# Kernel tuning notes

Measured on AMD Instinct MI355X. Metric: run time of the kernel, lower is better.

Reference implementation:

```python
import jax, jax.numpy as jnp
import numpy as np

D_MODEL = 512
D_FFN = 2048
N_LAYERS = 6
VOCAB = 1000
D_STATE = 16
D_CONV = 4
D_INNER = 2 * D_MODEL  # expand=2
DT_RANK = 32           # ceil(d_model/16)
B, LT, LS = 2, 512, 512


def _pos_encoding(length, d_model):
    pos = np.arange(length, dtype=np.float32)[:, None]
    div = np.exp(np.arange(0, d_model, 2, dtype=np.float32) * (-np.log(10000.0) / d_model))
    pe = np.zeros((length, d_model), np.float32)
    pe[:, 0::2] = np.sin(pos * div)
    pe[:, 1::2] = np.cos(pos * div)
    return jnp.asarray(pe)


def _layer_norm(x, g, b, eps=1e-6):
    m = x.mean(-1, keepdims=True)
    v = ((x - m) ** 2).mean(-1, keepdims=True)
    return (x - m) * jax.lax.rsqrt(v + eps) * g + b


def _mamba(x, in_w, conv_w, conv_b, xproj_w, dt_w, dt_b, A_log, Dskip, out_w):
    # x: (b, l, d_model)
    b, l, _ = x.shape
    xz = x @ in_w.T                                   # (b, l, 2*d_inner)
    xc, z = jnp.split(xz, 2, axis=-1)
    # causal depthwise conv over time
    xt = jnp.transpose(xc, (0, 2, 1))                 # (b, d_inner, l)
    xt = jnp.pad(xt, ((0, 0), (0, 0), (D_CONV - 1, 0)))
    xt = jax.lax.conv_general_dilated(
        xt, conv_w, window_strides=(1,), padding='VALID',
        feature_group_count=D_INNER, dimension_numbers=('NCH', 'OIH', 'NCH'))
    xc = jax.nn.silu(jnp.transpose(xt, (0, 2, 1)) + conv_b)  # (b, l, d_inner)
    dbl = xc @ xproj_w.T                              # (b, l, dt_rank + 2*n)
    dt, Bm, Cm = jnp.split(dbl, [DT_RANK, DT_RANK + D_STATE], axis=-1)
    dt = jax.nn.softplus(dt @ dt_w.T + dt_b)          # (b, l, d_inner)
    A = -jnp.exp(A_log)                               # (d_inner, n)

    def step(h, xs):
        dt_t, B_t, C_t, u_t = xs                      # (b,d),(b,n),(b,n),(b,d)
        dA = jnp.exp(dt_t[..., None] * A)             # (b, d, n)
        h = dA * h + (dt_t * u_t)[..., None] * B_t[:, None, :]
        y = jnp.einsum('bdn,bn->bd', h, C_t)
        return h, y

    h0 = jnp.zeros((b, D_INNER, D_STATE), x.dtype)
    xs = (jnp.swapaxes(dt, 0, 1), jnp.swapaxes(Bm, 0, 1),
          jnp.swapaxes(Cm, 0, 1), jnp.swapaxes(xc, 0, 1))
    _, ys = jax.lax.scan(step, h0, xs)                # ys: (l, b, d_inner)
    y = jnp.swapaxes(ys, 0, 1) + xc * Dskip
    y = y * jax.nn.silu(z)
    return y @ out_w.T                                # (b, l, d_model)


def setup_inputs() -> dict:
    key = jax.random.key(0)
    ks = iter(jax.random.split(key, 40))

    def rn(shape, s=0.02):
        return jax.random.normal(next(ks), shape, jnp.float32) * s

    def mamba_params():
        return dict(
            in_w=rn((N_LAYERS, 2 * D_INNER, D_MODEL)),
            conv_w=rn((N_LAYERS, D_INNER, 1, D_CONV), 0.1),
            conv_b=rn((N_LAYERS, D_INNER)),
            xproj=rn((N_LAYERS, DT_RANK + 2 * D_STATE, D_INNER)),
            dtw=rn((N_LAYERS, D_INNER, DT_RANK)),
            dtb=rn((N_LAYERS, D_INNER)),
            Alog=jnp.log(jnp.broadcast_to(jnp.arange(1.0, D_STATE + 1.0, dtype=jnp.float32), (N_LAYERS, D_INNER, D_STATE))),
            D=jnp.ones((N_LAYERS, D_INNER), jnp.float32),
            outw=rn((N_LAYERS, D_MODEL, D_INNER)),
        )

    ps, pc = mamba_params(), mamba_params()
    inp = {
        'src': jax.random.normal(next(ks), (B, LS, D_MODEL), jnp.float32),
        'tgt': jax.random.randint(next(ks), (B, LT), 0, VOCAB),
        'emb': rn((VOCAB, D_MODEL)),
        'in_w_s': ps['in_w'], 'conv_w_s': ps['conv_w'], 'conv_b_s': ps['conv_b'],
        'xproj_s': ps['xproj'], 'dtw_s': ps['dtw'], 'dtb_s': ps['dtb'],
        'Alog_s': ps['Alog'], 'D_s': ps['D'], 'outw_s': ps['outw'],
        'in_w_c': pc['in_w'], 'conv_w_c': pc['conv_w'], 'conv_b_c': pc['conv_b'],
        'xproj_c': pc['xproj'], 'dtw_c': pc['dtw'], 'dtb_c': pc['dtb'],
        'Alog_c': pc['Alog'], 'D_c': pc['D'], 'outw_c': pc['outw'],
        'ffn_w1': rn((N_LAYERS, D_FFN, D_MODEL)),
        'ffn_b1': jnp.zeros((N_LAYERS, D_FFN), jnp.float32),
        'ffn_w2': rn((N_LAYERS, D_MODEL, D_FFN)),
        'ffn_b2': jnp.zeros((N_LAYERS, D_MODEL), jnp.float32),
        'ln_g': jnp.ones((N_LAYERS, 3, D_MODEL), jnp.float32),
        'ln_b': jnp.zeros((N_LAYERS, 3, D_MODEL), jnp.float32),
        'fin_g': jnp.ones((D_MODEL,), jnp.float32),
        'fin_b': jnp.zeros((D_MODEL,), jnp.float32),
    }
    return inp


def reference(src, tgt, emb, in_w_s, conv_w_s, conv_b_s, xproj_s, dtw_s, dtb_s,
              Alog_s, D_s, outw_s, in_w_c, conv_w_c, conv_b_c, xproj_c, dtw_c,
              dtb_c, Alog_c, D_c, outw_c, ffn_w1, ffn_b1, ffn_w2, ffn_b2,
              ln_g, ln_b, fin_g, fin_b):
    # NormalizedEmbedding + sinusoidal positional encoding
    x = emb[tgt] * jnp.sqrt(jnp.asarray(D_MODEL, jnp.float32))
    x = x + _pos_encoding(LT, D_MODEL)[None]
    for i in range(N_LAYERS):
        # self mamba (post-norm, normalize_before=False)
        t2 = _mamba(x, in_w_s[i], conv_w_s[i], conv_b_s[i], xproj_s[i],
                    dtw_s[i], dtb_s[i], Alog_s[i], D_s[i], outw_s[i])
        x = _layer_norm(x + t2, ln_g[i, 0], ln_b[i, 0])
        # cross mamba over concat([memory, tgt]) then take last LT steps
        cat = jnp.concatenate([src, x], axis=1)
        t2 = _mamba(cat, in_w_c[i], conv_w_c[i], conv_b_c[i], xproj_c[i],
                    dtw_c[i], dtb_c[i], Alog_c[i], D_c[i], outw_c[i])[:, -LT:]
        x = _layer_norm(x + t2, ln_g[i, 1], ln_b[i, 1])
        # positionwise FFN
        h = jax.nn.relu(x @ ffn_w1[i].T + ffn_b1[i]) @ ffn_w2[i].T + ffn_b2[i]
        x = _layer_norm(x + h, ln_g[i, 2], ln_b[i, 2])
    return _layer_norm(x, fin_g, fin_b)
```

## Files before the change

kernel.cpp:

```cpp
#include <hip/hip_runtime.h>
#include <math.h>

#define DMODEL 512
#define DINNER 1024
#define DSTATE 16
#define DTRANK 32
#define NLAYERS 6
#define BB 2
#define LT 512
#define LS 512

typedef __attribute__((ext_vector_type(8))) short bf16x8;
typedef __attribute__((ext_vector_type(8))) unsigned short u16x8;
typedef __attribute__((ext_vector_type(4))) float f32x4;

__device__ __forceinline__ unsigned short f2bf(float f) {
  unsigned u = __float_as_uint(f);
  u += 0x7fffu + ((u >> 16) & 1u);
  return (unsigned short)(u >> 16);
}
__device__ __forceinline__ float bf2f(unsigned short u) {
  return __uint_as_float((unsigned)u << 16);
}

template<int EPI>
__device__ __forceinline__ float epi_apply(float acc, float b) {
  if (EPI == 1) { float v = acc + b; return v > 0.f ? v : 0.f; }
  if (EPI == 2) { return acc + b; }
  if (EPI == 3) { float v = acc + b; return fmaxf(v, 0.f) + log1pf(__expf(-fabsf(v))); }
  return acc;
}

__global__ __launch_bounds__(256) void cvt_all_kernel(
    const float* __restrict__ i0, const float* __restrict__ i1,
    const float* __restrict__ i2, const float* __restrict__ i3,
    const float* __restrict__ i4, const float* __restrict__ i5,
    const float* __restrict__ i6, const float* __restrict__ i7,
    const float* __restrict__ i8, const float* __restrict__ i9,
    unsigned short* __restrict__ outbase) {
  int i = blockIdx.x * 256 + threadIdx.x;
  if (i >= 8159232) return;
  const float* in; int off;
  if      (i < 1572864) { in = i0; off = i; }
  else if (i < 3145728) { in = i1; off = i - 1572864; }
  else if (i < 3244032) { in = i2; off = i - 3145728; }
  else if (i < 3342336) { in = i3; off = i - 3244032; }
  else if (i < 3391488) { in = i4; off = i - 3342336; }
  else if (i < 3440640) { in = i5; off = i - 3391488; }
  else if (i < 4227072) { in = i6; off = i - 3440640; }
  else if (i < 5013504) { in = i7; off = i - 4227072; }
  else if (i < 6586368) { in = i8; off = i - 5013504; }
  else                  { in = i9; off = i - 6586368; }
  float4 a = ((const float4*)in)[off];
  ushort4 o = make_ushort4(f2bf(a.x), f2bf(a.y), f2bf(a.z), f2bf(a.w));
  *(ushort4*)&outbase[(size_t)i * 4] = o;
}

__global__ __launch_bounds__(256) void embed_cat_kernel(const int* __restrict__ tgt,
    const float* __restrict__ emb, const float* __restrict__ src,
    float* __restrict__ X, unsigned short* __restrict__ Xb,
    unsigned short* __restrict__ CATb) {
  if (blockIdx.x < 2048) {
    int i = blockIdx.x * 256 + threadIdx.x;
    int d = i & (DMODEL - 1);
    int bt = i >> 9;
    int t = bt & (LT - 1);
    int tok = tgt[bt];
    float div = __expf((float)(d & ~1) * (-9.210340371976184f / (float)DMODEL));
    float ang = (float)t * div;
    float pe = (d & 1) ? cosf(ang) : sinf(ang);
    float v = emb[(size_t)tok * DMODEL + d] * 22.627416997969522f + pe;
    X[i] = v;
    Xb[i] = f2bf(v);
  } else {
    int i = (blockIdx.x - 2048) * 256 + threadIdx.x;
    int c8 = (i & 63) * 8;
    int r = i >> 6;
    int b = r >> 9, l = r & 511;
    const float* s = src + ((size_t)b * 512 + l) * DMODEL + c8;
    float4 a = *(const float4*)s;
    float4 bq = *(const float4*)(s + 4);
    u16x8 o;
    o[0] = f2bf(a.x); o[1] = f2bf(a.y); o[2] = f2bf(a.z); o[3] = f2bf(a.w);
    o[4] = f2bf(bq.x); o[5] = f2bf(bq.y); o[6] = f2bf(bq.z); o[7] = f2bf(bq.w);
    *(u16x8*)&CATb[((size_t)b * 1024 + l) * DMODEL + c8] = o;
  }
}

template<int BK, int EPI, bool SPLIT, bool OUTB>
__global__ __launch_bounds__(256) void mgemmA(
    const unsigned short* __restrict__ A, const unsigned short* __restrict__ Bw,
    const float* __restrict__ bias, float* __restrict__ C,
    unsigned short* __restrict__ Cb, int M, int N, int K, int lda) {
  constexpr int PAD = BK + 8;
  constexpr int CHA = BK / 32;
  constexpr int CHB = BK / 16;
  __shared__ __align__(16) unsigned short As[2][64 * PAD];
  __shared__ __align__(16) unsigned short Bs[2][128 * PAD];
  const int tid = threadIdx.x;
  const int bn = blockIdx.x * 128;
  const int bm = blockIdx.y * 64;
  const int lane = tid & 63;
  const int w = tid >> 6;
  const int wr = (w >> 1) * 32;
  const int wc = (w & 1) * 64;
  const int l15 = lane & 15;
  const int l4 = lane >> 4;
  const int koff = l4 * 8;
  int kcnt = K, kbeg = 0;
  if (SPLIT) { kcnt = K / (int)gridDim.z; kbeg = blockIdx.z * kcnt; }
  const int nt = kcnt / BK;
  f32x4 acc[2][4] = {};

  int arow_[CHA], ak8_[CHA];
  const unsigned short* Ap[CHA];
#pragma unroll
  for (int i = 0; i < CHA; ++i) {
    int f = tid + 256 * i;
    arow_[i] = f / (BK / 8);
    ak8_[i] = (f % (BK / 8)) * 8;
    Ap[i] = A + (size_t)(bm + arow_[i]) * lda + kbeg + ak8_[i];
  }
  int brow_[CHB], bk8_[CHB];
  const unsigned short* Bp[CHB];
#pragma unroll
  for (int i = 0; i < CHB; ++i) {
    int f = tid + 256 * i;
    brow_[i] = f / (BK / 8);
    bk8_[i] = (f % (BK / 8)) * 8;
    Bp[i] = Bw + (size_t)(bn + brow_[i]) * K + kbeg + bk8_[i];
  }

  u16x8 av[CHA], bv[CHB];
#pragma unroll
  for (int i = 0; i < CHA; ++i) av[i] = *(const u16x8*)Ap[i];
#pragma unroll
  for (int i = 0; i < CHB; ++i) bv[i] = *(const u16x8*)Bp[i];

  int cur = 0;
  for (int t = 0; t < nt; ++t) {
#pragma unroll
    for (int i = 0; i < CHA; ++i) *(u16x8*)&As[cur][arow_[i] * PAD + ak8_[i]] = av[i];
#pragma unroll
    for (int i = 0; i < CHB; ++i) *(u16x8*)&Bs[cur][brow_[i] * PAD + bk8_[i]] = bv[i];
    if (t + 1 < nt) {
      int ko = (t + 1) * BK;
#pragma unroll
      for (int i = 0; i < CHA; ++i) av[i] = *(const u16x8*)(Ap[i] + ko);
#pragma unroll
      for (int i = 0; i < CHB; ++i) bv[i] = *(const u16x8*)(Bp[i] + ko);
    }
    __syncthreads();
#pragma unroll
    for (int kk = 0; kk < BK / 32; ++kk) {
      bf16x8 afr[2], bfr[4];
#pragma unroll
      for (int i = 0; i < 2; ++i)
        afr[i] = *(const bf16x8*)&As[cur][(wr + i * 16 + l15) * PAD + kk * 32 + koff];
#pragma unroll
      for (int j = 0; j < 4; ++j)
        bfr[j] = *(const bf16x8*)&Bs[cur][(wc + j * 16 + l15) * PAD + kk * 32 + koff];
#pragma unroll
      for (int fr = 0; fr < 2; ++fr)
#pragma unroll
        for (int fc = 0; fc < 4; ++fc)
          acc[fr][fc] = __builtin_amdgcn_mfma_f32_16x16x32_bf16(
              afr[fr], bfr[fc], acc[fr][fc], 0, 0, 0);
    }
    cur ^= 1;
  }

  if (SPLIT) {
    unsigned short* Pz = Cb + (size_t)blockIdx.z * M * N;
#pragma unroll
    for (int fc = 0; fc < 4; ++fc) {
      int col = bn + wc + fc * 16 + l15;
#pragma unroll
      for (int fr = 0; fr < 2; ++fr) {
        int row0 = bm + wr + fr * 16 + l4 * 4;
#pragma unroll
        for (int r = 0; r < 4; ++r)
          Pz[(size_t)(row0 + r) * N + col] = f2bf(acc[fr][fc][r]);
      }
    }
  } else {
#pragma unroll
    for (int fc = 0; fc < 4; ++fc) {
      int col = bn + wc + fc * 16 + l15;
      float bvs = (EPI != 0) ? bias[col] : 0.f;
#pragma unroll
      for (int fr = 0; fr < 2; ++fr) {
        int row0 = bm + wr + fr * 16 + l4 * 4;
#pragma unroll
        for (int r = 0; r < 4; ++r) {
          float v = epi_apply<EPI>(acc[fr][fc][r], bvs);
          if (OUTB) Cb[(size_t)(row0 + r) * N + col] = f2bf(v);
          else      C[(size_t)(row0 + r) * N + col] = v;
        }
      }
    }
  }
}

template<int BK, int EPI, bool SPLIT, bool OUTB>
__global__ __launch_bounds__(256) void mgemm(
    const unsigned short* __restrict__ A, const unsigned short* __restrict__ Bw,
    const float* __restrict__ bias, float* __restrict__ C,
    unsigned short* __restrict__ Cb, int M, int N, int K, int lda) {
  constexpr int PAD = BK + 8;
  constexpr int CH = BK / 32;
  __shared__ __align__(16) unsigned short As[2][64 * PAD];
  __shared__ __align__(16) unsigned short Bs[2][64 * PAD];
  const int tid = threadIdx.x;
  const int bn = blockIdx.x * 64;
  const int bm = blockIdx.y * 64;
  const int lane = tid & 63;
  const int w = tid >> 6;
  const int wr = (w >> 1) * 32;
  const int wc = (w & 1) * 32;
  const int l15 = lane & 15;
  const int l4 = lane >> 4;
  const int koff = l4 * 8;
  int kcnt = K, kbeg = 0;
  if (SPLIT) { kcnt = K / (int)gridDim.z; kbeg = blockIdx.z * kcnt; }
  const int nt = kcnt / BK;
  f32x4 acc[2][2] = {};

  int row_[CH], k8_[CH];
  const unsigned short *Ap[CH], *Bp[CH];
#pragma unroll
  for (int i = 0; i < CH; ++i) {
    int f = tid + 256 * i;
    row_[i] = f / (BK / 8);
    k8_[i] = (f % (BK / 8)) * 8;
    Ap[i] = A + (size_t)(bm + row_[i]) * lda + kbeg + k8_[i];
    Bp[i] = Bw + (size_t)(bn + row_[i]) * K + kbeg + k8_[i];
  }

  u16x8 av[CH], bv[CH];
#pragma unroll
  for (int i = 0; i < CH; ++i) { av[i] = *(const u16x8*)Ap[i]; bv[i] = *(const u16x8*)Bp[i]; }

  int cur = 0;
  for (int t = 0; t < nt; ++t) {
#pragma unroll
    for (int i = 0; i < CH; ++i) {
      *(u16x8*)&As[cur][row_[i] * PAD + k8_[i]] = av[i];
      *(u16x8*)&Bs[cur][row_[i] * PAD + k8_[i]] = bv[i];
    }
    if (t + 1 < nt) {
      int ko = (t + 1) * BK;
#pragma unroll
      for (int i = 0; i < CH; ++i) {
        av[i] = *(const u16x8*)(Ap[i] + ko);
        bv[i] = *(const u16x8*)(Bp[i] + ko);
      }
    }
    __syncthreads();
#pragma unroll
    for (int kk = 0; kk < CH; ++kk) {
      bf16x8 afr[2], bfr[2];
#pragma unroll
      for (int i = 0; i < 2; ++i) {
        afr[i] = *(const bf16x8*)&As[cur][(wr + i * 16 + l15) * PAD + kk * 32 + koff];
        bfr[i] = *(const bf16x8*)&Bs[cur][(wc + i * 16 + l15) * PAD + kk * 32 + koff];
      }
#pragma unroll
      for (int fr = 0; fr < 2; ++fr)
#pragma unroll
        for (int fc = 0; fc < 2; ++fc)
          acc[fr][fc] = __builtin_amdgcn_mfma_f32_16x16x32_bf16(
              afr[fr], bfr[fc], acc[fr][fc], 0, 0, 0);
    }
    cur ^= 1;
  }

  if (SPLIT) {
    float* Pz = C + (size_t)blockIdx.z * M * N;
#pragma unroll
    for (int fc = 0; fc < 2; ++fc) {
      int col = bn + wc + fc * 16 + l15;
#pragma unroll
      for (int fr = 0; fr < 2; ++fr) {
        int row0 = bm + wr + fr * 16 + l4 * 4;
#pragma unroll
        for (int r = 0; r < 4; ++r)
          Pz[(size_t)(row0 + r) * N + col] = acc[fr][fc][r];
      }
    }
  } else {
#pragma unroll
    for (int fc = 0; fc < 2; ++fc) {
      int col = bn + wc + fc * 16 + l15;
      float bvs = (EPI != 0) ? bias[col] : 0.f;
#pragma unroll
      for (int fr = 0; fr < 2; ++fr) {
        int row0 = bm + wr + fr * 16 + l4 * 4;
#pragma unroll
        for (int r = 0; r < 4; ++r) {
          float v = epi_apply<EPI>(acc[fr][fc][r], bvs);
          if (OUTB) Cb[(size_t)(row0 + r) * N + col] = f2bf(v);
          else      C[(size_t)(row0 + r) * N + col] = v;
        }
      }
    }
  }
}

__global__ __launch_bounds__(256) void conv_silu_kernel(
    const unsigned short* __restrict__ xzb, const float* __restrict__ w,
    const float* __restrict__ bias, unsigned short* __restrict__ outb, int L) {
  int idx = blockIdx.x * 256 + threadIdx.x;
  int d8 = (idx & 127) * 8;
  int bt = idx >> 7;
  int b = bt / L;
  int t = bt - b * L;
  const unsigned short* col = xzb + ((size_t)b * L) * (2 * DINNER) + d8;
  float acc[8];
  float4 wv[8];
#pragma unroll
  for (int j = 0; j < 8; ++j) {
    acc[j] = bias[d8 + j];
    wv[j] = *(const float4*)(w + (size_t)(d8 + j) * 4);
  }
#pragma unroll
  for (int k = 0; k < 4; ++k) {
    int tt = t - 3 + k;
    if (tt >= 0) {
      u16x8 v = *(const u16x8*)(col + (size_t)tt * (2 * DINNER));
      float wk[8] = {
        k == 0 ? wv[0].x : k == 1 ? wv[0].y : k == 2 ? wv[0].z : wv[0].w,
        k == 0 ? wv[1].x : k == 1 ? wv[1].y : k == 2 ? wv[1].z : wv[1].w,
        k == 0 ? wv[2].x : k == 1 ? wv[2].y : k == 2 ? wv[2].z : wv[2].w,
        k == 0 ? wv[3].x : k == 1 ? wv[3].y : k == 2 ? wv[3].z : wv[3].w,
        k == 0 ? wv[4].x : k == 1 ? wv[4].y : k == 2 ? wv[4].z : wv[4].w,
        k == 0 ? wv[5].x : k == 1 ? wv[5].y : k == 2 ? wv[5].z : wv[5].w,
        k == 0 ? wv[6].x : k == 1 ? wv[6].y : k == 2 ? wv[6].z : wv[6].w,
        k == 0 ? wv[7].x : k == 1 ? wv[7].y : k == 2 ? wv[7].z : wv[7].w };
#pragma unroll
      for (int j = 0; j < 8; ++j) acc[j] = fmaf(bf2f(v[j]), wk[j], acc[j]);
    }
  }
  u16x8 o;
#pragma unroll
  for (int j = 0; j < 8; ++j) {
    float sig = 1.f / (1.f + __expf(-acc[j]));
    o[j] = f2bf(acc[j] * sig);
  }
  *(u16x8*)&outb[(size_t)bt * DINNER + d8] = o;
}

__global__ __launch_bounds__(256) void scan_pass1(
    const float* __restrict__ XPP, const unsigned short* __restrict__ u,
    const float* __restrict__ Alog, const float* __restrict__ dtw,
    const float* __restrict__ dtb, float* __restrict__ P, float* __restrict__ S,
    int L, int CL) {
  __shared__ float DBL8[32][64];
  const int tid = threadIdx.x;
  const int d = blockIdx.x * 256 + tid;
  const int b = blockIdx.y;
  const int c = blockIdx.z;
  const int t0 = c * CL;
  if (tid < CL * 8) {
    int t = tid >> 3, j8 = (tid & 7) * 8;
    const float* p = XPP + ((size_t)b * L + t0 + t) * 64 + j8;
    const size_t zs = (size_t)BB * L * 64;
    float s[8] = {0.f, 0.f, 0.f, 0.f, 0.f, 0.f, 0.f, 0.f};
#pragma unroll
    for (int z = 0; z < 8; ++z) {
      float4 a = *(const float4*)(p + z * zs);
      float4 bq = *(const float4*)(p + z * zs + 4);
      s[0] += a.x; s[1] += a.y; s[2] += a.z; s[3] += a.w;
      s[4] += bq.x; s[5] += bq.y; s[6] += bq.z; s[7] += bq.w;
    }
#pragma unroll
    for (int j = 0; j < 8; ++j) DBL8[t][j8 + j] = s[j];
  }
  float A[16];
#pragma unroll
  for (int j = 0; j < 4; ++j) {
    float4 a4 = *(const float4*)(Alog + d * 16 + j * 4);
    A[j * 4 + 0] = -__expf(a4.x); A[j * 4 + 1] = -__expf(a4.y);
    A[j * 4 + 2] = -__expf(a4.z); A[j * 4 + 3] = -__expf(a4.w);
  }
  float wreg[32];
#pragma unroll
  for (int j = 0; j < 8; ++j) {
    float4 w4 = *(const float4*)(dtw + (size_t)d * 32 + j * 4);
    wreg[j*4+0] = w4.x; wreg[j*4+1] = w4.y; wreg[j*4+2] = w4.z; wreg[j*4+3] = w4.w;
  }
  float dtbv = dtb[d];
  float h[16], Pp[16];
#pragma unroll
  for (int n = 0; n < 16; ++n) { h[n] = 0.f; Pp[n] = 1.f; }
  const unsigned short* up = u + ((size_t)b * L + t0) * DINNER + d;
  __syncthreads();
  for (int t = 0; t < CL; ++t) {
    float dtraw = dtbv;
#pragma unroll
    for (int k8 = 0; k8 < 8; ++k8) {
      float4 q = *(const float4*)&DBL8[t][k8 * 4];
      dtraw = fmaf(q.x, wreg[k8*4+0], dtraw);
      dtraw = fmaf(q.y, wreg[k8*4+1], dtraw);
      dtraw = fmaf(q.z, wreg[k8*4+2], dtraw);
      dtraw = fmaf(q.w, wreg[k8*4+3], dtraw);
    }
    float dtv = fmaxf(dtraw, 0.f) + log1pf(__expf(-fabsf(dtraw)));
    float uv = bf2f(up[(size_t)t * DINNER]);
    float du = dtv * uv;
    float Bv[16];
#pragma unroll
    for (int j = 0; j < 4; ++j) {
      float4 b4 = *(const float4*)&DBL8[t][32 + j * 4];
      Bv[j*4+0] = b4.x; Bv[j*4+1] = b4.y; Bv[j*4+2] = b4.z; Bv[j*4+3] = b4.w;
    }
#pragma unroll
    for (int n = 0; n < 16; ++n) {
      float dA = __expf(dtv * A[n]);
      Pp[n] *= dA;
      h[n] = fmaf(dA, h[n], du * Bv[n]);
    }
  }
  size_t base = (size_t)c * 32768 + ((size_t)(b * 1024 + d) << 4);
#pragma unroll
  for (int j = 0; j < 4; ++j) {
    *(float4*)&P[base + j * 4] = make_float4(Pp[j*4], Pp[j*4+1], Pp[j*4+2], Pp[j*4+3]);
    *(float4*)&S[base + j * 4] = make_float4(h[j*4], h[j*4+1], h[j*4+2], h[j*4+3]);
  }
}

__global__ __launch_bounds__(256) void scan_pass2(
    const float* __restrict__ XPP, const unsigned short* __restrict__ u,
    const unsigned short* __restrict__ xzb, const float* __restrict__ Alog,
    const float* __restrict__ dtw, const float* __restrict__ dtb,
    const float* __restrict__ Dsk, const float* __restrict__ P,
    const float* __restrict__ S, unsigned short* __restrict__ ysb,
    int L, int CL, int c0) {
  __shared__ float DBL8[32][64];
  const int tid = threadIdx.x;
  const int d = blockIdx.x * 256 + tid;
  const int b = blockIdx.y;
  const int c = blockIdx.z + c0;
  const int t0 = c * CL;
  if (tid < CL * 8) {
    int t = tid >> 3, j8 = (tid & 7) * 8;
    const float* p = XPP + ((size_t)b * L + t0 + t) * 64 + j8;
    const size_t zs = (size_t)BB * L * 64;
    float s[8] = {0.f, 0.f, 0.f, 0.f, 0.f, 0.f, 0.f, 0.f};
#pragma unroll
    for (int z = 0; z < 8; ++z) {
      float4 a = *(const float4*)(p + z * zs);
      float4 bq = *(const float4*)(p + z * zs + 4);
      s[0] += a.x; s[1] += a.y; s[2] += a.z; s[3] += a.w;
      s[4] += bq.x; s[5] += bq.y; s[6] += bq.z; s[7] += bq.w;
    }
#pragma unroll
    for (int j = 0; j < 8; ++j) DBL8[t][j8 + j] = s[j];
  }
  float A[16];
#pragma unroll
  for (int j = 0; j < 4; ++j) {
    float4 a4 = *(const float4*)(Alog + d * 16 + j * 4);
    A[j * 4 + 0] = -__expf(a4.x); A[j * 4 + 1] = -__expf(a4.y);
    A[j * 4 + 2] = -__expf(a4.z); A[j * 4 + 3] = -__expf(a4.w);
  }
  float wreg[32];
#pragma unroll
  for (int j = 0; j < 8; ++j) {
    float4 w4 = *(const float4*)(dtw + (size_t)d * 32 + j * 4);
    wreg[j*4+0] = w4.x; wreg[j*4+1] = w4.y; wreg[j*4+2] = w4.z; wreg[j*4+3] = w4.w;
  }
  float dtbv = dtb[d];
  float h[16];
#pragma unroll
  for (int n = 0; n < 16; ++n) h[n] = 0.f;
  size_t sbase = (size_t)(b * 1024 + d) << 4;
  for (int cc = 0; cc < c; ++cc) {
    size_t bb = (size_t)cc * 32768 + sbase;
#pragma unroll
    for (int j = 0; j < 4; ++j) {
      float4 p4 = *(const float4*)&P[bb + j * 4];
      float4 s4 = *(const float4*)&S[bb + j * 4];
      h[j*4+0] = fmaf(p4.x, h[j*4+0], s4.x);
      h[j*4+1] = fmaf(p4.y, h[j*4+1], s4.y);
      h[j*4+2] = fmaf(p4.z, h[j*4+2], s4.z);
      h[j*4+3] = fmaf(p4.w, h[j*4+3], s4.w);
    }
  }
  float Dv = Dsk[d];
  const unsigned short* up = u + ((size_t)b * L + t0) * DINNER + d;
  const unsigned short* zp = xzb + ((size_t)b * L + t0) * (2 * DINNER) + DINNER + d;
  unsigned short* yp = ysb + ((size_t)(b * 512) + (t0 - c0 * CL)) * DINNER + d;
  __syncthreads();
  for (int t = 0; t < CL; ++t) {
    float dtraw = dtbv;
#pragma unroll
    for (int k8 = 0; k8 < 8; ++k8) {
      float4 q = *(const float4*)&DBL8[t][k8 * 4];
      dtraw = fmaf(q.x, wreg[k8*4+0], dtraw);
      dtraw = fmaf(q.y, wreg[k8*4+1], dtraw);
      dtraw = fmaf(q.z, wreg[k8*4+2], dtraw);
      dtraw = fmaf(q.w, wreg[k8*4+3], dtraw);
    }
    float dtv = fmaxf(dtraw, 0.f) + log1pf(__expf(-fabsf(dtraw)));
    float uv = bf2f(up[(size_t)t * DINNER]);
    float zv = bf2f(zp[(size_t)t * (2 * DINNER)]);
    float du = dtv * uv;
    float Bv[16], Cv[16];
#pragma unroll
    for (int j = 0; j < 4; ++j) {
      float4 b4 = *(const float4*)&DBL8[t][32 + j * 4];
      float4 c4 = *(const float4*)&DBL8[t][48 + j * 4];
      Bv[j*4+0] = b4.x; Bv[j*4+1] = b4.y; Bv[j*4+2] = b4.z; Bv[j*4+3] = b4.w;
      Cv[j*4+0] = c4.x; Cv[j*4+1] = c4.y; Cv[j*4+2] = c4.z; Cv[j*4+3] = c4.w;
    }
    float y = 0.f;
#pragma unroll
    for (int n = 0; n < 16; ++n) {
      float dA = __expf(dtv * A[n]);
      h[n] = fmaf(dA, h[n], du * Bv[n]);
      y = fmaf(h[n], Cv[n], y);
    }
    float sig = 1.f / (1.f + __expf(-zv));
    yp[(size_t)t * DINNER] = f2bf((y + uv * Dv) * (zv * sig));
  }
}

template<int NZ, int EPI, bool FIN>
__global__ __launch_bounds__(64) void ln_red_kernel(
    const float* __restrict__ res, const unsigned short* __restrict__ Pb,
    const float* __restrict__ bias, const float* __restrict__ g,
    const float* __restrict__ be, float* __restrict__ out,
    unsigned short* __restrict__ outb, int row_scale, int row_off,
    const float* __restrict__ fing, const float* __restrict__ finb,
    float* __restrict__ fout) {
  int r = blockIdx.x;
  int b = r >> 9, t = r & 511;
  int lane = threadIdx.x;
  const float* rp = res + (size_t)r * DMODEL;
  size_t ob = ((size_t)(b * row_scale + row_off + t)) * DMODEL;
  float v[8];
  float s = 0.f, ss = 0.f;
#pragma unroll
  for (int j = 0; j < 8; ++j) {
    int col = lane + j * 64;
    float acc = 0.f;
#pragma unroll
    for (int z = 0; z < NZ; ++z)
      acc += bf2f(Pb[(size_t)z * 524288 + (size_t)r * DMODEL + col]);
    float bv = (EPI != 0) ? bias[col] : 0.f;
    float x = rp[col] + epi_apply<EPI>(acc, bv);
    v[j] = x; s += x; ss += x * x;
  }
#pragma unroll
  for (int o = 32; o > 0; o >>= 1) { s += __shfl_xor(s, o); ss += __shfl_xor(ss, o); }
  float m = s * (1.f / 512.f);
  float var = ss * (1.f / 512.f) - m * m;
  float rs = rsqrtf(var + 1e-6f);
  if (FIN) {
    float o2[8];
    float s2 = 0.f, ss2 = 0.f;
#pragma unroll
    for (int j = 0; j < 8; ++j) {
      int col = lane + j * 64;
      float x = (v[j] - m) * rs * g[col] + be[col];
      o2[j] = x; s2 += x; ss2 += x * x;
    }
#pragma unroll
    for (int o = 32; o > 0; o >>= 1) { s2 += __shfl_xor(s2, o); ss2 += __shfl_xor(ss2, o); }
    float m2 = s2 * (1.f / 512.f);
    float var2 = ss2 * (1.f / 512.f) - m2 * m2;
    float rs2 = rsqrtf(var2 + 1e-6f);
#pragma unroll
    for (int j = 0; j < 8; ++j) {
      int col = lane + j * 64;
      fout[(size_t)r * DMODEL + col] = (o2[j] - m2) * rs2 * fing[col] + finb[col];
    }
  } else {
#pragma unroll
    for (int j = 0; j < 8; ++j) {
      int col = lane + j * 64;
      float o2 = (v[j] - m) * rs * g[col] + be[col];
      out[(size_t)r * DMODEL + col] = o2;
      outb[ob + col] = f2bf(o2);
    }
  }
}

extern "C" void kernel_launch(void* const* d_in, const int* in_sizes, int n_in,
                              void* d_out, int out_size, void* d_ws, size_t ws_size,
                              hipStream_t stream) {
  (void)in_sizes; (void)n_in; (void)out_size; (void)ws_size;
  const float* src      = (const float*)d_in[0];
  const int*   tgt      = (const int*)d_in[1];
  const float* emb      = (const float*)d_in[2];
  const float* in_w_s   = (const float*)d_in[3];
  const float* conv_w_s = (const float*)d_in[4];
  const float* conv_b_s = (const float*)d_in[5];
  const float* xproj_s  = (const float*)d_in[6];
  const float* dtw_s    = (const float*)d_in[7];
  const float* dtb_s    = (const float*)d_in[8];
  const float* Alog_s   = (const float*)d_in[9];
  const float* D_s      = (const float*)d_in[10];
  const float* outw_s   = (const float*)d_in[11];
  const float* in_w_c   = (const float*)d_in[12];
  const float* conv_w_c = (const float*)d_in[13];
  const float* conv_b_c = (const float*)d_in[14];
  const float* xproj_c  = (const float*)d_in[15];
  const float* dtw_c    = (const float*)d_in[16];
  const float* dtb_c    = (const float*)d_in[17];
  const float* Alog_c   = (const float*)d_in[18];
  const float* D_c      = (const float*)d_in[19];
  const float* outw_c   = (const float*)d_in[20];
  const float* ffn_w1   = (const float*)d_in[21];
  const float* ffn_b1   = (const float*)d_in[22];
  const float* ffn_w2   = (const float*)d_in[23];
  const float* ffn_b2   = (const float*)d_in[24];
  const float* ln_g     = (const float*)d_in[25];
  const float* ln_b     = (const float*)d_in[26];
  const float* fin_g    = (const float*)d_in[27];
  const float* fin_b    = (const float*)d_in[28];

  float* ws   = (float*)d_ws;
  float* X    = ws;
  float* XPP  = X + 524288;
  float* SC_P = XPP + 1048576;
  float* SC_S = SC_P + 1048576;
  unsigned short* U = (unsigned short*)(SC_S + 1048576);
  unsigned short* Xb   = U;
  unsigned short* CATb = Xb + 524288;
  unsigned short* XCb  = CATb + 1048576;
  unsigned short* XZb  = XCb + 2097152;
  unsigned short* YSb  = XZb + 4194304;
  unsigned short* XZPb = YSb + 1048576;
  unsigned short* WB   = XZPb + 4194304;
  unsigned short* inwsb = WB;
  unsigned short* inwcb = inwsb + 6291456;
  unsigned short* xpsb  = inwcb + 6291456;
  unsigned short* xpcb  = xpsb + 393216;
  unsigned short* dtwsb = xpcb + 393216;
  unsigned short* dtwcb = dtwsb + 196608;
  unsigned short* owsb  = dtwcb + 196608;
  unsigned short* owcb  = owsb + 3145728;
  unsigned short* f1b   = owcb + 3145728;
  unsigned short* f2b   = f1b + 6291456;

  cvt_all_kernel<<<31872, 256, 0, stream>>>(
      in_w_s, in_w_c, xproj_s, xproj_c, dtw_s, dtw_c, outw_s, outw_c,
      ffn_w1, ffn_w2, WB);
  embed_cat_kernel<<<2304, 256, 0, stream>>>(tgt, emb, src, X, Xb, CATb);

  for (int i = 0; i < NLAYERS; ++i) {
    mgemm<64, 0, false, true><<<dim3(32, 16), 256, 0, stream>>>(
        Xb, inwsb + (size_t)i * 1048576, nullptr, nullptr, XZb, 1024, 2048, 512, 512);
    conv_silu_kernel<<<512, 256, 0, stream>>>(
        XZb, conv_w_s + (size_t)i * 4096, conv_b_s + (size_t)i * 1024, XCb, 512);
    mgemm<64, 0, true, false><<<dim3(1, 16, 8), 256, 0, stream>>>(
        XCb, xpsb + (size_t)i * 65536, nullptr, XPP, nullptr, 1024, 64, 1024, 1024);
    scan_pass1<<<dim3(4, 2, 32), 256, 0, stream>>>(
        XPP, XCb, Alog_s + (size_t)i * 16384, dtw_s + (size_t)i * 32768,
        dtb_s + (size_t)i * 1024, SC_P, SC_S, 512, 16);
    scan_pass2<<<dim3(4, 2, 32), 256, 0, stream>>>(
        XPP, XCb, XZb, Alog_s + (size_t)i * 16384, dtw_s + (size_t)i * 32768,
        dtb_s + (size_t)i * 1024, D_s + (size_t)i * 1024, SC_P, SC_S, YSb, 512, 16, 0);
    mgemmA<64, 0, true, false><<<dim3(4, 16, 8), 256, 0, stream>>>(
        YSb, owsb + (size_t)i * 524288, nullptr, nullptr, XZPb, 1024, 512, 1024, 1024);
    ln_red_kernel<8, 0, false><<<1024, 64, 0, stream>>>(
        X, XZPb, nullptr, ln_g + (size_t)(i * 3 + 0) * 512,
        ln_b + (size_t)(i * 3 + 0) * 512, X, CATb, 1024, 512,
        nullptr, nullptr, nullptr);

    mgemmA<64, 0, false, true><<<dim3(16, 32), 256, 0, stream>>>(
        CATb, inwcb + (size_t)i * 1048576, nullptr, nullptr, XZb, 2048, 2048, 512, 512);
    conv_silu_kernel<<<1024, 256, 0, stream>>>(
        XZb, conv_w_c + (size_t)i * 4096, conv_b_c + (size_t)i * 1024, XCb, 1024);
    mgemm<64, 0, true, false><<<dim3(1, 32, 8), 256, 0, stream>>>(
        XCb, xpcb + (size_t)i * 65536, nullptr, XPP, nullptr, 2048, 64, 1024, 1024);
    scan_pass1<<<dim3(4, 2, 32), 256, 0, stream>>>(
        XPP, XCb, Alog_c + (size_t)i * 16384, dtw_c + (size_t)i * 32768,
        dtb_c + (size_t)i * 1024, SC_P, SC_S, 1024, 32);
    scan_pass2<<<dim3(4, 2, 16), 256, 0, stream>>>(
        XPP, XCb, XZb, Alog_c + (size_t)i * 16384, dtw_c + (size_t)i * 32768,
        dtb_c + (size_t)i * 1024, D_c + (size_t)i * 1024, SC_P, SC_S, YSb, 1024, 32, 16);
    mgemmA<64, 0, true, false><<<dim3(4, 16, 8), 256, 0, stream>>>(
        YSb, owcb + (size_t)i * 524288, nullptr, nullptr, XZPb, 1024, 512, 1024, 1024);
    ln_red_kernel<8, 0, false><<<1024, 64, 0, stream>>>(
        X, XZPb, nullptr, ln_g + (size_t)(i * 3 + 1) * 512,
        ln_b + (size_t)(i * 3 + 1) * 512, X, Xb, 512, 0,
        nullptr, nullptr, nullptr);

    mgemm<64, 1, false, true><<<dim3(32, 16), 256, 0, stream>>>(
        Xb, f1b + (size_t)i * 1048576, ffn_b1 + (size_t)i * 2048, nullptr, XZb,
        1024, 2048, 512, 512);
    mgemmA<64, 0, true, false><<<dim3(4, 16, 8), 256, 0, stream>>>(
        XZb, f2b + (size_t)i * 1048576, nullptr, nullptr, XZPb, 1024, 512, 2048, 2048);
    if (i < NLAYERS - 1) {
      ln_red_kernel<8, 2, false><<<1024, 64, 0, stream>>>(
          X, XZPb, ffn_b2 + (size_t)i * 512, ln_g + (size_t)(i * 3 + 2) * 512,
          ln_b + (size_t)(i * 3 + 2) * 512, X, Xb, 512, 0,
          nullptr, nullptr, nullptr);
    } else {
      ln_red_kernel<8, 2, true><<<1024, 64, 0, stream>>>(
          X, XZPb, ffn_b2 + (size_t)i * 512, ln_g + (size_t)(i * 3 + 2) * 512,
          ln_b + (size_t)(i * 3 + 2) * 512, nullptr, nullptr, 512, 0,
          fin_g, fin_b, (float*)d_out);
    }
  }
}
```

Measured before the change: 1.137 ms.

## Merge weight-convert and embed kernels, pack LN rows per block, add nontemporal split-K I/O

Combines the weight bf16 conversion and the embedding/concat kernel into one launch to save a launch. Split-K partial stores and the layer-norm reductions' partial loads now use nontemporal hints. The layer-norm kernel handles four rows per 256-thread block instead of one row per 64-thread block, giving fewer, larger blocks. The nontemporal hints could hurt if the partials would otherwise have been served from cache.

```diff
diff --git a/kernel.cpp b/kernel.cpp
--- a/kernel.cpp
+++ b/kernel.cpp
@@ -31,37 +31,35 @@
   return acc;
 }
 
-__global__ __launch_bounds__(256) void cvt_all_kernel(
+__global__ __launch_bounds__(256) void cvt_embed_kernel(
     const float* __restrict__ i0, const float* __restrict__ i1,
     const float* __restrict__ i2, const float* __restrict__ i3,
     const float* __restrict__ i4, const float* __restrict__ i5,
     const float* __restrict__ i6, const float* __restrict__ i7,
     const float* __restrict__ i8, const float* __restrict__ i9,
-    unsigned short* __restrict__ outbase) {
-  int i = blockIdx.x * 256 + threadIdx.x;
-  if (i >= 8159232) return;
-  const float* in; int off;
-  if      (i < 1572864) { in = i0; off = i; }
-  else if (i < 3145728) { in = i1; off = i - 1572864; }
-  else if (i < 3244032) { in = i2; off = i - 3145728; }
-  else if (i < 3342336) { in = i3; off = i - 3244032; }
-  else if (i < 3391488) { in = i4; off = i - 3342336; }
-  else if (i < 3440640) { in = i5; off = i - 3391488; }
-  else if (i < 4227072) { in = i6; off = i - 3440640; }
-  else if (i < 5013504) { in = i7; off = i - 4227072; }
-  else if (i < 6586368) { in = i8; off = i - 5013504; }
-  else                  { in = i9; off = i - 6586368; }
-  float4 a = ((const float4*)in)[off];
-  ushort4 o = make_ushort4(f2bf(a.x), f2bf(a.y), f2bf(a.z), f2bf(a.w));
-  *(ushort4*)&outbase[(size_t)i * 4] = o;
-}
-
-__global__ __launch_bounds__(256) void embed_cat_kernel(const int* __restrict__ tgt,
-    const float* __restrict__ emb, const float* __restrict__ src,
-    float* __restrict__ X, unsigned short* __restrict__ Xb,
-    unsigned short* __restrict__ CATb) {
-  if (blockIdx.x < 2048) {
+    unsigned short* __restrict__ outbase,
+    const int* __restrict__ tgt, const float* __restrict__ emb,
+    const float* __restrict__ src, float* __restrict__ X,
+    unsigned short* __restrict__ Xb, unsigned short* __restrict__ CATb) {
+  if (blockIdx.x < 31872) {
     int i = blockIdx.x * 256 + threadIdx.x;
+    if (i >= 8159232) return;
+    const float* in; int off;
+    if      (i < 1572864) { in = i0; off = i; }
+    else if (i < 3145728) { in = i1; off = i - 1572864; }
+    else if (i < 3244032) { in = i2; off = i - 3145728; }
+    else if (i < 3342336) { in = i3; off = i - 3244032; }
+    else if (i < 3391488) { in = i4; off = i - 3342336; }
+    else if (i < 3440640) { in = i5; off = i - 3391488; }
+    else if (i < 4227072) { in = i6; off = i - 3440640; }
+    else if (i < 5013504) { in = i7; off = i - 4227072; }
+    else if (i < 6586368) { in = i8; off = i - 5013504; }
+    else                  { in = i9; off = i - 6586368; }
+    float4 a = ((const float4*)in)[off];
+    ushort4 o = make_ushort4(f2bf(a.x), f2bf(a.y), f2bf(a.z), f2bf(a.w));
+    *(ushort4*)&outbase[(size_t)i * 4] = o;
+  } else if (blockIdx.x < 31872 + 2048) {
+    int i = (blockIdx.x - 31872) * 256 + threadIdx.x;
     int d = i & (DMODEL - 1);
     int bt = i >> 9;
     int t = bt & (LT - 1);
@@ -73,7 +71,7 @@
     X[i] = v;
     Xb[i] = f2bf(v);
   } else {
-    int i = (blockIdx.x - 2048) * 256 + threadIdx.x;
+    int i = (blockIdx.x - 31872 - 2048) * 256 + threadIdx.x;
     int c8 = (i & 63) * 8;
     int r = i >> 6;
     int b = r >> 9, l = r & 511;
@@ -180,7 +178,8 @@
         int row0 = bm + wr + fr * 16 + l4 * 4;
 #pragma unroll
         for (int r = 0; r < 4; ++r)
-          Pz[(size_t)(row0 + r) * N + col] = f2bf(acc[fr][fc][r]);
+          __builtin_nontemporal_store(f2bf(acc[fr][fc][r]),
+                                      &Pz[(size_t)(row0 + r) * N + col]);
       }
     }
   } else {
@@ -285,7 +284,8 @@
         int row0 = bm + wr + fr * 16 + l4 * 4;
 #pragma unroll
         for (int r = 0; r < 4; ++r)
-          Pz[(size_t)(row0 + r) * N + col] = acc[fr][fc][r];
+          __builtin_nontemporal_store(acc[fr][fc][r],
+                                      &Pz[(size_t)(row0 + r) * N + col]);
       }
     }
   } else {
@@ -527,16 +527,16 @@
 }
 
 template<int NZ, int EPI, bool FIN>
-__global__ __launch_bounds__(64) void ln_red_kernel(
+__global__ __launch_bounds__(256) void ln_red_kernel(
     const float* __restrict__ res, const unsigned short* __restrict__ Pb,
     const float* __restrict__ bias, const float* __restrict__ g,
     const float* __restrict__ be, float* __restrict__ out,
     unsigned short* __restrict__ outb, int row_scale, int row_off,
     const float* __restrict__ fing, const float* __restrict__ finb,
     float* __restrict__ fout) {
-  int r = blockIdx.x;
+  int r = blockIdx.x * 4 + (threadIdx.x >> 6);
   int b = r >> 9, t = r & 511;
-  int lane = threadIdx.x;
+  int lane = threadIdx.x & 63;
   const float* rp = res + (size_t)r * DMODEL;
   size_t ob = ((size_t)(b * row_scale + row_off + t)) * DMODEL;
   float v[8];
@@ -547,7 +547,8 @@
     float acc = 0.f;
 #pragma unroll
     for (int z = 0; z < NZ; ++z)
-      acc += bf2f(Pb[(size_t)z * 524288 + (size_t)r * DMODEL + col]);
+      acc += bf2f(__builtin_nontemporal_load(
+          &Pb[(size_t)z * 524288 + (size_t)r * DMODEL + col]));
     float bv = (EPI != 0) ? bias[col] : 0.f;
     float x = rp[col] + epi_apply<EPI>(acc, bv);
     v[j] = x; s += x; ss += x * x;
@@ -645,10 +646,9 @@
   unsigned short* f1b   = owcb + 3145728;
   unsigned short* f2b   = f1b + 6291456;
 
-  cvt_all_kernel<<<31872, 256, 0, stream>>>(
+  cvt_embed_kernel<<<34176, 256, 0, stream>>>(
       in_w_s, in_w_c, xproj_s, xproj_c, dtw_s, dtw_c, outw_s, outw_c,
-      ffn_w1, ffn_w2, WB);
-  embed_cat_kernel<<<2304, 256, 0, stream>>>(tgt, emb, src, X, Xb, CATb);
+      ffn_w1, ffn_w2, WB, tgt, emb, src, X, Xb, CATb);
 
   for (int i = 0; i < NLAYERS; ++i) {
     mgemm<64, 0, false, true><<<dim3(32, 16), 256, 0, stream>>>(
@@ -665,7 +665,7 @@
         dtb_s + (size_t)i * 1024, D_s + (size_t)i * 1024, SC_P, SC_S, YSb, 512, 16, 0);
     mgemmA<64, 0, true, false><<<dim3(4, 16, 8), 256, 0, stream>>>(
         YSb, owsb + (size_t)i * 524288, nullptr, nullptr, XZPb, 1024, 512, 1024, 1024);
-    ln_red_kernel<8, 0, false><<<1024, 64, 0, stream>>>(
+    ln_red_kernel<8, 0, false><<<256, 256, 0, stream>>>(
         X, XZPb, nullptr, ln_g + (size_t)(i * 3 + 0) * 512,
         ln_b + (size_t)(i * 3 + 0) * 512, X, CATb, 1024, 512,
         nullptr, nullptr, nullptr);
@@ -684,7 +684,7 @@
         dtb_c + (size_t)i * 1024, D_c + (size_t)i * 1024, SC_P, SC_S, YSb, 1024, 32, 16);
     mgemmA<64, 0, true, false><<<dim3(4, 16, 8), 256, 0, stream>>>(
         YSb, owcb + (size_t)i * 524288, nullptr, nullptr, XZPb, 1024, 512, 1024, 1024);
-    ln_red_kernel<8, 0, false><<<1024, 64, 0, stream>>>(
+    ln_red_kernel<8, 0, false><<<256, 256, 0, stream>>>(
         X, XZPb, nullptr, ln_g + (size_t)(i * 3 + 1) * 512,
         ln_b + (size_t)(i * 3 + 1) * 512, X, Xb, 512, 0,
         nullptr, nullptr, nullptr);
@@ -695,12 +695,12 @@
     mgemmA<64, 0, true, false><<<dim3(4, 16, 8), 256, 0, stream>>>(
         XZb, f2b + (size_t)i * 1048576, nullptr, nullptr, XZPb, 1024, 512, 2048, 2048);
     if (i < NLAYERS - 1) {
-      ln_red_kernel<8, 2, false><<<1024, 64, 0, stream>>>(
+      ln_red_kernel<8, 2, false><<<256, 256, 0, stream>>>(
           X, XZPb, ffn_b2 + (size_t)i * 512, ln_g + (size_t)(i * 3 + 2) * 512,
           ln_b + (size_t)(i * 3 + 2) * 512, X, Xb, 512, 0,
           nullptr, nullptr, nullptr);
     } else {
-      ln_red_kernel<8, 2, true><<<1024, 64, 0, stream>>>(
+      ln_red_kernel<8, 2, true><<<256, 256, 0, stream>>>(
           X, XZPb, ffn_b2 + (size_t)i * 512, ln_g + (size_t)(i * 3 + 2) * 512,
           ln_b + (size_t)(i * 3 + 2) * 512, nullptr, nullptr, 512, 0,
           fin_g, fin_b, (float*)d_out);
```

After: 1.190 ms. +4.6%, slower.
